# Kernel tuning notes

Measured on AMD Instinct MI355X. Metric: run time of the kernel, lower is better.

Reference implementation:

```python
import jax, jax.numpy as jnp
import numpy as np

D_MODEL, N_HEADS, D_K = 768, 12, 64
LN_EPS = 1e-5


def setup_inputs() -> dict:
    key = jax.random.key(0)
    ks = jax.random.split(key, 8)
    b, c, n, s = 8, 32, 4, 64
    scale = 1.0 / np.sqrt(D_MODEL)
    inp = {
        "e": jax.random.normal(ks[0], (b, c, n, s, D_MODEL), dtype=jnp.float32),
        "h": jax.random.normal(ks[1], (b, c, s, D_MODEL), dtype=jnp.float32),
        # weights stored [in, out] (torch Linear transposed)
        "Wq": jax.random.normal(ks[2], (D_MODEL, N_HEADS * D_K), dtype=jnp.float32) * scale,
        "bq": jnp.zeros((N_HEADS * D_K,), dtype=jnp.float32),
        "Wk": jax.random.normal(ks[3], (D_MODEL, N_HEADS * D_K), dtype=jnp.float32) * scale,
        "bk": jnp.zeros((N_HEADS * D_K,), dtype=jnp.float32),
        "Wv": jax.random.normal(ks[4], (D_MODEL, N_HEADS * D_K), dtype=jnp.float32) * scale,
        "bv": jnp.zeros((N_HEADS * D_K,), dtype=jnp.float32),
        "Wo": jax.random.normal(ks[5], (N_HEADS * D_K, D_MODEL), dtype=jnp.float32) * scale,
        "bo": jnp.zeros((D_MODEL,), dtype=jnp.float32),
        "ln_g": jnp.ones((D_MODEL,), dtype=jnp.float32),
        "ln_b": jnp.zeros((D_MODEL,), dtype=jnp.float32),
    }
    return inp


def _layer_norm(x, g, b):
    mu = jnp.mean(x, axis=-1, keepdims=True)
    var = jnp.mean(jnp.square(x - mu), axis=-1, keepdims=True)
    return (x - mu) * jax.lax.rsqrt(var + LN_EPS) * g + b


def reference(e, h, Wq, bq, Wk, bk, Wv, bv, Wo, bo, ln_g, ln_b):
    # e: [b, c, n, i, d]  h: [b, c, j, d]
    e_res = e
    en = _layer_norm(e, ln_g, ln_b)
    b, c, n, i, _ = e.shape
    j = h.shape[2]
    q = (en @ Wq + bq).reshape(b, c, n, i, N_HEADS, D_K)
    k = (h @ Wk + bk).reshape(b, c, j, N_HEADS, D_K)
    v = (h @ Wv + bv).reshape(b, c, j, N_HEADS, D_K)
    attn = jnp.einsum('bcnihd,bcjhd->bcnhij', q, k) * (1.0 / np.sqrt(D_K))
    attn = jax.nn.softmax(attn, axis=-1)
    o = jnp.einsum('bcnhij,bcjhd->bcnihd', attn, v).reshape(b, c, n, i, N_HEADS * D_K)
    return o @ Wo + bo + e_res
```

## Files before the change

### kernel.cpp

```cpp
#include <hip/hip_runtime.h>

typedef __bf16 bf16x8 __attribute__((ext_vector_type(8)));
typedef __bf16 bf16x4 __attribute__((ext_vector_type(4)));
typedef float f32x4 __attribute__((ext_vector_type(4)));

__device__ __forceinline__ f32x4 mfma16(bf16x8 a, bf16x8 b, f32x4 c) {
  return __builtin_amdgcn_mfma_f32_16x16x32_bf16(a, b, c, 0, 0, 0);
}

__device__ __forceinline__ void load_lds16(const void* g, void* l) {
  __builtin_amdgcn_global_load_lds(
      (const __attribute__((address_space(1))) void*)g,
      (__attribute__((address_space(3))) void*)l, 16, 0, 0);
}

template <int NWG>
__device__ __forceinline__ int xcd_swz(int orig) {
  constexpr int NX = 8;
  constexpr int q = NWG / NX;
  constexpr int r = NWG % NX;
  const int xcd = orig % NX;
  const int pos = orig / NX;
  if constexpr (r == 0) {
    return xcd * q + pos;
  } else {
    return (xcd < r ? xcd * (q + 1) : r * (q + 1) + (xcd - r) * q) + pos;
  }
}

__global__ __launch_bounds__(256) void prep_w_kernel(
    const float* __restrict__ Wq, const float* __restrict__ Wk,
    const float* __restrict__ Wv, const float* __restrict__ Wo,
    __bf16* __restrict__ WqT, __bf16* __restrict__ WkvT, __bf16* __restrict__ WoT) {
  __shared__ float tile[32][33];
  const int z = blockIdx.z;
  const float* W = (z == 0) ? Wq : (z == 1) ? Wk : (z == 2) ? Wv : Wo;
  __bf16* out = (z == 0) ? WqT : (z == 3) ? WoT : WkvT;
  const int rowOff = (z == 2) ? 768 : 0;
  const int tx = threadIdx.x, ty = threadIdx.y;
  const int x = blockIdx.x * 32 + tx;
  const int y = blockIdx.y * 32 + ty;
#pragma unroll
  for (int i = 0; i < 32; i += 8) tile[ty + i][tx] = W[(size_t)(y + i) * 768 + x];
  __syncthreads();
  const int nx = blockIdx.y * 32 + tx;
  const int ny = blockIdx.x * 32 + ty;
#pragma unroll
  for (int i = 0; i < 32; i += 8)
    out[(size_t)(rowOff + ny + i) * 768 + nx] = (__bf16)tile[tx][ty + i];
}

__global__ __launch_bounds__(256) void ln_kernel(
    const float* __restrict__ e, const float* __restrict__ gam,
    const float* __restrict__ bet, __bf16* __restrict__ en) {
  const int lane = threadIdx.x & 63;
  const int wid = threadIdx.x >> 6;
  const size_t row = (size_t)blockIdx.x * 4 + wid;
  const float* p = e + row * 768;
  float x[12];
  float sum = 0.f;
#pragma unroll
  for (int s = 0; s < 3; ++s) {
    f32x4 v = *(const f32x4*)(p + (s * 64 + lane) * 4);
#pragma unroll
    for (int q = 0; q < 4; ++q) { x[s * 4 + q] = v[q]; sum += v[q]; }
  }
#pragma unroll
  for (int d = 1; d < 64; d <<= 1) sum += __shfl_xor(sum, d);
  const float m = sum * (1.f / 768.f);
  float vs = 0.f;
#pragma unroll
  for (int q = 0; q < 12; ++q) { float d = x[q] - m; vs += d * d; }
#pragma unroll
  for (int d = 1; d < 64; d <<= 1) vs += __shfl_xor(vs, d);
  const float rr = rsqrtf(vs * (1.f / 768.f) + 1e-5f);
  __bf16* o = en + row * 768;
#pragma unroll
  for (int s = 0; s < 3; ++s) {
    f32x4 g4 = *(const f32x4*)(gam + (s * 64 + lane) * 4);
    f32x4 b4 = *(const f32x4*)(bet + (s * 64 + lane) * 4);
    bf16x4 pk;
#pragma unroll
    for (int q = 0; q < 4; ++q) pk[q] = (__bf16)((x[s * 4 + q] - m) * rr * g4[q] + b4[q]);
    *(bf16x4*)(o + (s * 64 + lane) * 4) = pk;
  }
}

__global__ __launch_bounds__(256) void cast_kernel(
    const float* __restrict__ in, __bf16* __restrict__ out, int n4) {
  int i = blockIdx.x * 256 + threadIdx.x;
  const int stride = gridDim.x * 256;
  for (; i < n4; i += stride) {
    f32x4 v = ((const f32x4*)in)[i];
    bf16x4 o;
#pragma unroll
    for (int q = 0; q < 4; ++q) o[q] = (__bf16)v[q];
    ((bf16x4*)out)[i] = o;
  }
}

enum { MODE_Q = 0, MODE_KV = 1, MODE_O = 2 };

template <int MODE, int NC, int NWG>
__global__ __launch_bounds__(512) void gemm8_kernel(
    const __bf16* __restrict__ A,
    const __bf16* __restrict__ WT,
    const float* __restrict__ bias0, const float* __restrict__ bias1,
    const float* __restrict__ eres,
    __bf16* __restrict__ dst0, __bf16* __restrict__ dst1,
    float* __restrict__ outp) {
  __shared__ __bf16 As[4 * 8192];
  __shared__ __bf16 Bs[4 * 8192];
  const int wgid = xcd_swz<NWG>(blockIdx.x);
  const int rowBase = (wgid / NC) * 256;
  const int colBase = (wgid % NC) * 256;
  const int t = threadIdx.x;
  const int lane = t & 63, wid = t >> 6;
  const int wm = wid >> 2, wn = wid & 3;
  const int lr = lane & 15, lg = lane >> 4;
  const int srow = t >> 2;
  const int skcol = ((t & 3) ^ (srow & 3)) * 8;
  const int cg = lg ^ (lr & 3);
  f32x4 acc[8][4] = {};

  auto stageA = [&](int kt) {
    const int slot = kt & 3;
#pragma unroll
    for (int p = 0; p < 2; ++p) {
      const int rowIn = p * 128 + srow;
      const __bf16* ga;
      if constexpr (MODE == MODE_O) {
        const int r = rowBase + rowIn;
        ga = A + ((((size_t)(r >> 6)) * 12 + (kt >> 1)) << 12) + ((r & 63) << 6) +
             (kt & 1) * 32 + skcol;
      } else {
        ga = A + (size_t)(rowBase + rowIn) * 768 + kt * 32 + skcol;
      }
      load_lds16(ga, &As[slot * 8192 + p * 4096 + t * 8]);
    }
  };
  auto stageB = [&](int kt) {
    const int slot = kt & 3;
#pragma unroll
    for (int p = 0; p < 2; ++p) {
      const int rowIn = p * 128 + srow;
      const __bf16* gb = WT + (size_t)(colBase + rowIn) * 768 + kt * 32 + skcol;
      load_lds16(gb, &Bs[slot * 8192 + p * 4096 + t * 8]);
    }
  };

  stageA(0); stageB(0);
  stageA(1); stageB(1);
  stageA(2); stageB(2);

#pragma unroll
  for (int kt = 0; kt < 24; ++kt) {
    const int slot = kt & 3;
    if (kt <= 21) {
      asm volatile("s_waitcnt vmcnt(8)" ::: "memory");
    } else if (kt == 22) {
      asm volatile("s_waitcnt vmcnt(4)" ::: "memory");
    } else {
      asm volatile("s_waitcnt vmcnt(0)" ::: "memory");
    }
    __builtin_amdgcn_sched_barrier(0);
    __builtin_amdgcn_s_barrier();

    bf16x8 b[4], a0[4];
#pragma unroll
    for (int it = 0; it < 4; ++it)
      a0[it] = *(const bf16x8*)&As[slot * 8192 + (wm * 128 + it * 16 + lr) * 32 + cg * 8];
#pragma unroll
    for (int jt = 0; jt < 4; ++jt)
      b[jt] = *(const bf16x8*)&Bs[slot * 8192 + (wn * 64 + jt * 16 + lr) * 32 + cg * 8];
    if (kt + 3 < 24) stageA(kt + 3);
    asm volatile("s_waitcnt lgkmcnt(0)" ::: "memory");
    __builtin_amdgcn_sched_barrier(0);
    __builtin_amdgcn_s_setprio(1);
#pragma unroll
    for (int it = 0; it < 4; ++it)
#pragma unroll
      for (int jt = 0; jt < 4; ++jt)
        acc[it][jt] = mfma16(a0[it], b[jt], acc[it][jt]);
    __builtin_amdgcn_s_setprio(0);
    __builtin_amdgcn_s_barrier();

    bf16x8 a1[4];
#pragma unroll
    for (int it = 0; it < 4; ++it)
      a1[it] = *(const bf16x8*)&As[slot * 8192 + (wm * 128 + (it + 4) * 16 + lr) * 32 + cg * 8];
    if (kt + 3 < 24) stageB(kt + 3);
    asm volatile("s_waitcnt lgkmcnt(0)" ::: "memory");
    __builtin_amdgcn_sched_barrier(0);
    __builtin_amdgcn_s_setprio(1);
#pragma unroll
    for (int it = 0; it < 4; ++it)
#pragma unroll
      for (int jt = 0; jt < 4; ++jt)
        acc[it + 4][jt] = mfma16(a1[it], b[jt], acc[it + 4][jt]);
    __builtin_amdgcn_s_setprio(0);
  }

  const int roww = rowBase + wm * 128;
  const int colw = colBase + wn * 64;
#pragma unroll
  for (int it = 0; it < 8; ++it) {
#pragma unroll
    for (int jt = 0; jt < 4; ++jt) {
      const int c = colw + jt * 16 + lr;
#pragma unroll
      for (int rg = 0; rg < 4; ++rg) {
        const int r = roww + it * 16 + lg * 4 + rg;
        const float val = acc[it][jt][rg];
        if constexpr (MODE == MODE_O) {
          outp[(size_t)r * 768 + c] = val + bias0[c] + eres[(size_t)r * 768 + c];
        } else if constexpr (MODE == MODE_Q) {
          dst0[((((size_t)(r >> 6)) * 12 + (c >> 6)) << 12) + ((r & 63) << 6) + (c & 63)] =
              (__bf16)(val + bias0[c]);
        } else {
          if (c < 768) {
            dst0[((((size_t)(r >> 6)) * 12 + (c >> 6)) << 12) + ((r & 63) << 6) + (c & 63)] =
                (__bf16)(val + bias0[c]);
          } else {
            const int c2 = c - 768;
            dst1[((((size_t)(r >> 6)) * 12 + (c2 >> 6)) << 12) + ((c2 & 63) << 6) + (r & 63)] =
                (__bf16)(val + bias1[c2]);
          }
        }
      }
    }
  }
}

__global__ __launch_bounds__(256) void attn_kernel(
    const __bf16* __restrict__ q, const __bf16* __restrict__ k,
    const __bf16* __restrict__ v, __bf16* __restrict__ o) {
  const int bh = blockIdx.x;
  const int h = bh % 12;
  const int bc = bh / 12;
  const int t = threadIdx.x;
  const int wid = t >> 6, lane = t & 63;
  const int lr = lane & 15, lg = lane >> 4;
  __shared__ __bf16 kL[64][72];
  __shared__ __bf16 vL[64][72];
  __shared__ __bf16 P[4][64][72];

  {
    const __bf16* kp = k + ((size_t)bh << 12);
    const __bf16* vp = v + ((size_t)bh << 12);
    const int row = t >> 2, col = (t & 3) * 16;
    *(bf16x8*)&kL[row][col]     = *(const bf16x8*)(kp + row * 64 + col);
    *(bf16x8*)&kL[row][col + 8] = *(const bf16x8*)(kp + row * 64 + col + 8);
    *(bf16x8*)&vL[row][col]     = *(const bf16x8*)(vp + row * 64 + col);
    *(bf16x8*)&vL[row][col + 8] = *(const bf16x8*)(vp + row * 64 + col + 8);
  }
  const __bf16* qp = q + (((size_t)(bc * 4 + wid) * 12 + h) << 12);
  __bf16* op = o + (((size_t)(bc * 4 + wid) * 12 + h) << 12);
  bf16x8 qf[4][2];
#pragma unroll
  for (int it = 0; it < 4; ++it)
#pragma unroll
    for (int kc = 0; kc < 2; ++kc)
      qf[it][kc] = *(const bf16x8*)(qp + (it * 16 + lr) * 64 + kc * 32 + lg * 8);
  __syncthreads();

  f32x4 s[4][4] = {};
#pragma unroll
  for (int kc = 0; kc < 2; ++kc) {
    bf16x8 kf[4];
#pragma unroll
    for (int jt = 0; jt < 4; ++jt)
      kf[jt] = *(const bf16x8*)&kL[jt * 16 + lr][kc * 32 + lg * 8];
#pragma unroll
    for (int jt = 0; jt < 4; ++jt)
#pragma unroll
      for (int it = 0; it < 4; ++it)
        s[jt][it] = mfma16(kf[jt], qf[it][kc], s[jt][it]);
  }

  float recip[4];
#pragma unroll
  for (int it = 0; it < 4; ++it) {
    float m = -1e30f;
#pragma unroll
    for (int jt = 0; jt < 4; ++jt)
#pragma unroll
      for (int rg = 0; rg < 4; ++rg) m = fmaxf(m, s[jt][it][rg]);
    m = fmaxf(m, __shfl_xor(m, 16));
    m = fmaxf(m, __shfl_xor(m, 32));
    float sum = 0.f;
#pragma unroll
    for (int jt = 0; jt < 4; ++jt) {
      bf16x4 pk;
#pragma unroll
      for (int rg = 0; rg < 4; ++rg) {
        float p = __expf((s[jt][it][rg] - m) * 0.125f);
        sum += p;
        pk[rg] = (__bf16)p;
      }
      *(bf16x4*)&P[wid][it * 16 + lr][jt * 16 + lg * 4] = pk;
    }
    sum += __shfl_xor(sum, 16);
    sum += __shfl_xor(sum, 32);
    recip[it] = 1.f / sum;
  }

  f32x4 oacc[4][4] = {};
#pragma unroll
  for (int kc = 0; kc < 2; ++kc) {
    bf16x8 vf[4], pf[4];
#pragma unroll
    for (int dt = 0; dt < 4; ++dt)
      vf[dt] = *(const bf16x8*)&vL[dt * 16 + lr][kc * 32 + lg * 8];
#pragma unroll
    for (int it = 0; it < 4; ++it)
      pf[it] = *(const bf16x8*)&P[wid][it * 16 + lr][kc * 32 + lg * 8];
#pragma unroll
    for (int dt = 0; dt < 4; ++dt)
#pragma unroll
      for (int it = 0; it < 4; ++it)
        oacc[dt][it] = mfma16(vf[dt], pf[it], oacc[dt][it]);
  }
#pragma unroll
  for (int it = 0; it < 4; ++it) {
    const float rc = recip[it];
#pragma unroll
    for (int dt = 0; dt < 4; ++dt) {
      bf16x4 pk;
#pragma unroll
      for (int rg = 0; rg < 4; ++rg) pk[rg] = (__bf16)(oacc[dt][it][rg] * rc);
      *(bf16x4*)(op + (size_t)(it * 16 + lr) * 64 + dt * 16 + lg * 4) = pk;
    }
  }
}

extern "C" void kernel_launch(void* const* d_in, const int* in_sizes, int n_in,
                              void* d_out, int out_size, void* d_ws, size_t ws_size,
                              hipStream_t stream) {
  const float* e  = (const float*)d_in[0];
  const float* h  = (const float*)d_in[1];
  const float* Wq = (const float*)d_in[2];
  const float* bq = (const float*)d_in[3];
  const float* Wk = (const float*)d_in[4];
  const float* bk = (const float*)d_in[5];
  const float* Wv = (const float*)d_in[6];
  const float* bv = (const float*)d_in[7];
  const float* Wo = (const float*)d_in[8];
  const float* bo = (const float*)d_in[9];
  const float* g  = (const float*)d_in[10];
  const float* b  = (const float*)d_in[11];
  float* outp = (float*)d_out;
  char* ws = (char*)d_ws;

  __bf16* WqT  = (__bf16*)(ws);
  __bf16* WkvT = (__bf16*)(ws + 1179648);
  __bf16* WoT  = (__bf16*)(ws + 3538944);
  char* R1 = ws + 4718592;
  __bf16* en    = (__bf16*)(R1);
  __bf16* h_bf  = (__bf16*)(R1);
  __bf16* k_ws  = (__bf16*)(R1 + 25165824);
  __bf16* v_ws  = (__bf16*)(R1 + 50331648);
  __bf16* q_ws  = (__bf16*)(ws + 105381888);

  prep_w_kernel<<<dim3(24, 24, 4), dim3(32, 8), 0, stream>>>(Wq, Wk, Wv, Wo, WqT, WkvT, WoT);
  ln_kernel<<<16384, 256, 0, stream>>>(e, g, b, en);
  gemm8_kernel<MODE_Q, 3, 768><<<768, 512, 0, stream>>>(
      en, WqT, bq, nullptr, nullptr, q_ws, nullptr, nullptr);
  cast_kernel<<<2048, 256, 0, stream>>>(h, h_bf, 16384 * 768 / 4);
  gemm8_kernel<MODE_KV, 6, 384><<<384, 512, 0, stream>>>(
      h_bf, WkvT, bk, bv, nullptr, k_ws, v_ws, nullptr);
  attn_kernel<<<3072, 256, 0, stream>>>(q_ws, k_ws, v_ws, q_ws);
  gemm8_kernel<MODE_O, 3, 768><<<768, 512, 0, stream>>>(
      q_ws, WoT, bo, nullptr, e, nullptr, nullptr, outp);
}
```

Baseline: 481.6 us.

## Restructure attention to loop over heads per block with register prefetch

After: 486.2 us. Within noise of the previous version (+1.0%).

```diff
diff --git a/kernel.cpp b/kernel.cpp
--- a/kernel.cpp
+++ b/kernel.cpp
@@ -235,57 +235,62 @@
 __global__ __launch_bounds__(256) void attn_kernel(
     const __bf16* __restrict__ q, const __bf16* __restrict__ k,
     const __bf16* __restrict__ v, __bf16* __restrict__ o) {
-  const int bh = blockIdx.x;
-  const int h = bh % 12;
-  const int bc = bh / 12;
+  __shared__ __bf16 kL[64][72];
+  __shared__ __bf16 vL[64][72];
+  __shared__ __bf16 P[4][16][72];
+  const int bcn = xcd_swz<1024>(blockIdx.x);
+  const int bc = bcn >> 2;
   const int t = threadIdx.x;
   const int wid = t >> 6, lane = t & 63;
   const int lr = lane & 15, lg = lane >> 4;
-  __shared__ __bf16 kL[64][72];
-  __shared__ __bf16 vL[64][72];
-  __shared__ __bf16 P[4][64][72];
-
-  {
-    const __bf16* kp = k + ((size_t)bh << 12);
-    const __bf16* vp = v + ((size_t)bh << 12);
-    const int row = t >> 2, col = (t & 3) * 16;
-    *(bf16x8*)&kL[row][col]     = *(const bf16x8*)(kp + row * 64 + col);
-    *(bf16x8*)&kL[row][col + 8] = *(const bf16x8*)(kp + row * 64 + col + 8);
-    *(bf16x8*)&vL[row][col]     = *(const bf16x8*)(vp + row * 64 + col);
-    *(bf16x8*)&vL[row][col + 8] = *(const bf16x8*)(vp + row * 64 + col + 8);
-  }
-  const __bf16* qp = q + (((size_t)(bc * 4 + wid) * 12 + h) << 12);
-  __bf16* op = o + (((size_t)(bc * 4 + wid) * 12 + h) << 12);
-  bf16x8 qf[4][2];
-#pragma unroll
-  for (int it = 0; it < 4; ++it)
-#pragma unroll
-    for (int kc = 0; kc < 2; ++kc)
-      qf[it][kc] = *(const bf16x8*)(qp + (it * 16 + lr) * 64 + kc * 32 + lg * 8);
+  const __bf16* qbase = q + (size_t)bcn * 49152;
+  const __bf16* kbase = k + (size_t)bc * 49152;
+  const __bf16* vbase = v + (size_t)bc * 49152;
+  __bf16* obase = o + (size_t)bcn * 49152;
+  const int srow = t >> 3, scol = (t & 7) * 8;
+
+#pragma unroll
+  for (int s = 0; s < 2; ++s) {
+    *(bf16x8*)&kL[s * 32 + srow][scol] = *(const bf16x8*)(kbase + (s * 32 + srow) * 64 + scol);
+    *(bf16x8*)&vL[s * 32 + srow][scol] = *(const bf16x8*)(vbase + (s * 32 + srow) * 64 + scol);
+  }
+  bf16x8 qf[2];
+#pragma unroll
+  for (int kc = 0; kc < 2; ++kc)
+    qf[kc] = *(const bf16x8*)(qbase + (wid * 16 + lr) * 64 + kc * 32 + lg * 8);
   __syncthreads();
 
-  f32x4 s[4][4] = {};
-#pragma unroll
-  for (int kc = 0; kc < 2; ++kc) {
-    bf16x8 kf[4];
+  for (int h = 0; h < 12; ++h) {
+    bf16x8 kn[2], vn[2], qn[2];
+    if (h < 11) {
+      const __bf16* kp = kbase + (h + 1) * 4096;
+      const __bf16* vp = vbase + (h + 1) * 4096;
+      const __bf16* qp = qbase + (h + 1) * 4096;
+#pragma unroll
+      for (int s = 0; s < 2; ++s) {
+        kn[s] = *(const bf16x8*)(kp + (s * 32 + srow) * 64 + scol);
+        vn[s] = *(const bf16x8*)(vp + (s * 32 + srow) * 64 + scol);
+      }
+#pragma unroll
+      for (int kc = 0; kc < 2; ++kc)
+        qn[kc] = *(const bf16x8*)(qp + (wid * 16 + lr) * 64 + kc * 32 + lg * 8);
+    }
+    f32x4 s4[4] = {};
+#pragma unroll
+    for (int kc = 0; kc < 2; ++kc) {
+      bf16x8 kf[4];
+#pragma unroll
+      for (int jt = 0; jt < 4; ++jt)
+        kf[jt] = *(const bf16x8*)&kL[jt * 16 + lr][kc * 32 + lg * 8];
+#pragma unroll
+      for (int jt = 0; jt < 4; ++jt)
+        s4[jt] = mfma16(kf[jt], qf[kc], s4[jt]);
+    }
+    float m = -1e30f;
 #pragma unroll
     for (int jt = 0; jt < 4; ++jt)
-      kf[jt] = *(const bf16x8*)&kL[jt * 16 + lr][kc * 32 + lg * 8];
-#pragma unroll
-    for (int jt = 0; jt < 4; ++jt)
-#pragma unroll
-      for (int it = 0; it < 4; ++it)
-        s[jt][it] = mfma16(kf[jt], qf[it][kc], s[jt][it]);
-  }
-
-  float recip[4];
-#pragma unroll
-  for (int it = 0; it < 4; ++it) {
-    float m = -1e30f;
-#pragma unroll
-    for (int jt = 0; jt < 4; ++jt)
-#pragma unroll
-      for (int rg = 0; rg < 4; ++rg) m = fmaxf(m, s[jt][it][rg]);
+#pragma unroll
+      for (int rg = 0; rg < 4; ++rg) m = fmaxf(m, s4[jt][rg]);
     m = fmaxf(m, __shfl_xor(m, 16));
     m = fmaxf(m, __shfl_xor(m, 32));
     float sum = 0.f;
@@ -294,43 +299,45 @@
       bf16x4 pk;
 #pragma unroll
       for (int rg = 0; rg < 4; ++rg) {
-        float p = __expf((s[jt][it][rg] - m) * 0.125f);
+        float p = __expf((s4[jt][rg] - m) * 0.125f);
         sum += p;
         pk[rg] = (__bf16)p;
       }
-      *(bf16x4*)&P[wid][it * 16 + lr][jt * 16 + lg * 4] = pk;
+      *(bf16x4*)&P[wid][lr][jt * 16 + lg * 4] = pk;
     }
     sum += __shfl_xor(sum, 16);
     sum += __shfl_xor(sum, 32);
-    recip[it] = 1.f / sum;
-  }
-
-  f32x4 oacc[4][4] = {};
-#pragma unroll
-  for (int kc = 0; kc < 2; ++kc) {
-    bf16x8 vf[4], pf[4];
-#pragma unroll
-    for (int dt = 0; dt < 4; ++dt)
-      vf[dt] = *(const bf16x8*)&vL[dt * 16 + lr][kc * 32 + lg * 8];
-#pragma unroll
-    for (int it = 0; it < 4; ++it)
-      pf[it] = *(const bf16x8*)&P[wid][it * 16 + lr][kc * 32 + lg * 8];
-#pragma unroll
-    for (int dt = 0; dt < 4; ++dt)
-#pragma unroll
-      for (int it = 0; it < 4; ++it)
-        oacc[dt][it] = mfma16(vf[dt], pf[it], oacc[dt][it]);
-  }
-#pragma unroll
-  for (int it = 0; it < 4; ++it) {
-    const float rc = recip[it];
+    const float recip = 1.f / sum;
+    f32x4 oacc[4] = {};
+#pragma unroll
+    for (int kc = 0; kc < 2; ++kc) {
+      bf16x8 pf = *(const bf16x8*)&P[wid][lr][kc * 32 + lg * 8];
+      bf16x8 vf[4];
+#pragma unroll
+      for (int dt = 0; dt < 4; ++dt)
+        vf[dt] = *(const bf16x8*)&vL[dt * 16 + lr][kc * 32 + lg * 8];
+#pragma unroll
+      for (int dt = 0; dt < 4; ++dt)
+        oacc[dt] = mfma16(vf[dt], pf, oacc[dt]);
+    }
+    __bf16* op = obase + h * 4096;
 #pragma unroll
     for (int dt = 0; dt < 4; ++dt) {
       bf16x4 pk;
 #pragma unroll
-      for (int rg = 0; rg < 4; ++rg) pk[rg] = (__bf16)(oacc[dt][it][rg] * rc);
-      *(bf16x4*)(op + (size_t)(it * 16 + lr) * 64 + dt * 16 + lg * 4) = pk;
-    }
+      for (int rg = 0; rg < 4; ++rg) pk[rg] = (__bf16)(oacc[dt][rg] * recip);
+      *(bf16x4*)(op + (size_t)(wid * 16 + lr) * 64 + dt * 16 + lg * 4) = pk;
+    }
+    __syncthreads();
+    if (h < 11) {
+#pragma unroll
+      for (int s = 0; s < 2; ++s) {
+        *(bf16x8*)&kL[s * 32 + srow][scol] = kn[s];
+        *(bf16x8*)&vL[s * 32 + srow][scol] = vn[s];
+      }
+      qf[0] = qn[0]; qf[1] = qn[1];
+    }
+    __syncthreads();
   }
 }
 
@@ -369,7 +376,7 @@
   cast_kernel<<<2048, 256, 0, stream>>>(h, h_bf, 16384 * 768 / 4);
   gemm8_kernel<MODE_KV, 6, 384><<<384, 512, 0, stream>>>(
       h_bf, WkvT, bk, bv, nullptr, k_ws, v_ws, nullptr);
-  attn_kernel<<<3072, 256, 0, stream>>>(q_ws, k_ws, v_ws, q_ws);
+  attn_kernel<<<1024, 256, 0, stream>>>(q_ws, k_ws, v_ws, q_ws);
   gemm8_kernel<MODE_O, 3, 768><<<768, 512, 0, stream>>>(
       q_ws, WoT, bo, nullptr, e, nullptr, nullptr, outp);
 }
```
